# Optimization experiments

Measured on AMD Instinct MI355X. Metric: run time of the kernel, lower is better.

## Reference

```python
import jax, jax.numpy as jnp
import numpy as np

VOC_SIZE = 40
VOC_EMB = 32
LAYERS = [512, 1024, 2048]
LATENT = 512
START_TOK = 39
STOP_TOK = 0
MAX_STEPS = 50
BATCH = 64


def _gru_cell(x, h, Kg, bg, Kc, bc):
    # TF-style GRU: gates = sigmoid([x,h]@Kg + bg) -> (r, z);
    # cand = tanh([x, r*h]@Kc + bc); h' = z*h + (1-z)*cand
    out = h.shape[-1]
    v = jax.nn.sigmoid(jnp.concatenate([x, h], axis=-1) @ Kg + bg)
    r, z = v[..., :out], v[..., out:]
    c = jnp.tanh(jnp.concatenate([x, r * h], axis=-1) @ Kc + bc)
    return z * h + (1.0 - z) * c


def setup_inputs() -> dict:
    key = jax.random.key(0)
    ks = jax.random.split(key, 16)
    s = 0.05
    inp = {
        'input_vecs': jax.random.normal(ks[0], (BATCH, LATENT), jnp.float32),
        'emb': jax.random.normal(ks[1], (VOC_SIZE, VOC_EMB), jnp.float32) * s,
        'dense_W': jax.random.normal(ks[2], (LATENT, sum(LAYERS)), jnp.float32) * s,
        'dense_b': jnp.zeros((sum(LAYERS),), jnp.float32),
        'dec_W': jax.random.normal(ks[3], (LAYERS[2], VOC_SIZE), jnp.float32) * s,
    }
    ins = [VOC_EMB, LAYERS[0], LAYERS[1]]
    for i in range(3):
        ci = ins[i] + LAYERS[i]
        inp[f'Kg{i}'] = jax.random.normal(ks[4 + 4 * i], (ci, 2 * LAYERS[i]), jnp.float32) * s
        inp[f'bg{i}'] = jnp.ones((2 * LAYERS[i],), jnp.float32)  # TF GRU gate bias init 1.0
        inp[f'Kc{i}'] = jax.random.normal(ks[5 + 4 * i], (ci, LAYERS[i]), jnp.float32) * s
        inp[f'bc{i}'] = jnp.zeros((LAYERS[i],), jnp.float32)
    return inp


def reference(input_vecs, emb, dense_W, dense_b, dec_W,
              Kg0, bg0, Kc0, bc0, Kg1, bg1, Kc1, bc1, Kg2, bg2, Kc2, bc2):
    y = input_vecs @ dense_W + dense_b                       # [B, 3584]
    h0 = y[:, :LAYERS[0]]
    h1 = y[:, LAYERS[0]:LAYERS[0] + LAYERS[1]]
    h2 = y[:, LAYERS[0] + LAYERS[1]:]
    B = input_vecs.shape[0]
    x0 = jnp.broadcast_to(emb[START_TOK], (B, VOC_EMB))      # <s> embedding
    done0 = jnp.zeros((B,), bool)

    def step(carry, _):
        x, h0, h1, h2, done = carry
        n0 = _gru_cell(x, h0, Kg0, bg0, Kc0, bc0)
        n1 = _gru_cell(n0, h1, Kg1, bg1, Kc1, bc1)
        n2 = _gru_cell(n1, h2, Kg2, bg2, Kc2, bc2)
        logits = n2 @ dec_W                                  # [B, 40]
        idx = jnp.argmax(logits, axis=-1)                    # greedy sample
        d = done[:, None]
        # freeze state & outputs once a sequence emitted the stop token
        h0 = jnp.where(d, h0, n0)
        h1 = jnp.where(d, h1, n1)
        h2 = jnp.where(d, h2, n2)
        logits = jnp.where(d, 0.0, logits)
        tok = jnp.where(done, STOP_TOK, idx)
        x = jnp.where(d, x, emb[idx])
        done = done | (idx == STOP_TOK)
        return (x, h0, h1, h2, done), (tok, logits)

    _, (toks, logits) = jax.lax.scan(step, (x0, h0, h1, h2, done0), None, length=MAX_STEPS)
    # toks: [T, B] -> [B, T]; logits: [T, B, V] -> [B, T, V]
    return jnp.transpose(toks).astype(jnp.int32), jnp.transpose(logits, (1, 0, 2))
```

## Files before the change

kernel.cpp:

```cpp
#include <hip/hip_runtime.h>
#include <math.h>

#define NBLK 256
#define TPB  512
#define KB   128
#define ATS  65
#define LDSF 8448

#define GC 0
#define GG 512
#define RC 1024
#define RG 1056
#define AB 1088
__device__ unsigned g_sync[1120];
__device__ int g_tok[64];
__device__ int g_done[64];
__device__ __attribute__((aligned(16))) float g_hA[64 * 3584];
__device__ __attribute__((aligned(16))) float g_hB[64 * 3584];
__device__ __attribute__((aligned(16))) float g_v0h[64 * 1024];
__device__ __attribute__((aligned(16))) float g_v1a[64 * 2048];
__device__ __attribute__((aligned(16))) float g_v1b[64 * 2048];
__device__ __attribute__((aligned(16))) float g_c1x[64 * 1024];
__device__ __attribute__((aligned(16))) float g_v2a[64 * 4096];
__device__ __attribute__((aligned(16))) float g_v2b[64 * 4096];
__device__ __attribute__((aligned(16))) float g_cnd2a[64 * 2048];
__device__ __attribute__((aligned(16))) float g_cnd2b[64 * 2048];
__device__ __attribute__((aligned(16))) float g_c2x[64 * 2048];
__device__ __attribute__((aligned(16))) float g_ekg[40 * 1024];
__device__ __attribute__((aligned(16))) float g_ekc[40 * 512];

__device__ __forceinline__ float sigf(float x) { return 1.0f / (1.0f + __expf(-x)); }
__device__ __forceinline__ float tanhf_(float x) {
  float ax = fabsf(x);
  float e  = __expf(-2.0f * ax);
  float r  = (1.0f - e) / (1.0f + e);
  return copysignf(r, x);
}

__device__ __forceinline__ unsigned armw(unsigned* p, unsigned v) {
  return __hip_atomic_fetch_add(p, v, __ATOMIC_RELAXED, __HIP_MEMORY_SCOPE_AGENT);
}

struct AccP {
  const float* p; int lda;
  __device__ __forceinline__ float4 ld(int r, int k) const {
    return *(const float4*)(p + (size_t)r * lda + k);
  }
};
struct AccH {
  const float* pn; const float* po; int off; int cut;
  __device__ __forceinline__ float4 ld(int r, int k) const {
    const float* b = (k < cut) ? pn : po;
    return *(const float4*)(b + (size_t)r * 3584 + off + k);
  }
};
struct AccRH0 {
  const float* v; const float* ek; const int* tk; const float* h;
  __device__ __forceinline__ float4 ld(int r, int k) const {
    int t = tk[r];
    float4 a  = *(const float4*)(v + (size_t)r * 1024 + k);
    float4 b  = *(const float4*)(ek + (size_t)t * 1024 + k);
    float4 hh = *(const float4*)(h + (size_t)r * 3584 + k);
    return make_float4(sigf(a.x + b.x) * hh.x, sigf(a.y + b.y) * hh.y,
                       sigf(a.z + b.z) * hh.z, sigf(a.w + b.w) * hh.w);
  }
};
struct AccR1 {
  const float* va; const float* vb; const float* h;
  __device__ __forceinline__ float4 ld(int r, int k) const {
    float4 a  = *(const float4*)(va + (size_t)r * 2048 + k);
    float4 b  = *(const float4*)(vb + (size_t)r * 2048 + k);
    float4 hh = *(const float4*)(h + (size_t)r * 3584 + k);
    return make_float4(sigf(a.x + b.x) * hh.x, sigf(a.y + b.y) * hh.y,
                       sigf(a.z + b.z) * hh.z, sigf(a.w + b.w) * hh.w);
  }
};
struct AccR2 {
  const float* va; const float* vb; const float* h;
  __device__ __forceinline__ float4 ld(int r, int k) const {
    float4 a  = *(const float4*)(va + (size_t)r * 4096 + k);
    float4 b  = *(const float4*)(vb + (size_t)r * 4096 + k);
    float4 hh = *(const float4*)(h + (size_t)r * 3584 + k);
    return make_float4(sigf(a.x + b.x) * hh.x, sigf(a.y + b.y) * hh.y,
                       sigf(a.z + b.z) * hh.z, sigf(a.w + b.w) * hh.w);
  }
};
template <class Inner> struct AccOff {
  Inner in; int base;
  __device__ __forceinline__ float4 ld(int r, int k) const { return in.ld(r, base + k); }
};

#define FMA8(J, AJ) \
  acc[J][0] = fmaf(AJ, wv0.x, acc[J][0]); acc[J][1] = fmaf(AJ, wv0.y, acc[J][1]); \
  acc[J][2] = fmaf(AJ, wv0.z, acc[J][2]); acc[J][3] = fmaf(AJ, wv0.w, acc[J][3]); \
  acc[J][4] = fmaf(AJ, wv1.x, acc[J][4]); acc[J][5] = fmaf(AJ, wv1.y, acc[J][5]); \
  acc[J][6] = fmaf(AJ, wv1.z, acc[J][6]); acc[J][7] = fmaf(AJ, wv1.w, acc[J][7]);

template <class AF, class EF>
__device__ __forceinline__ void gemm32(const AF& A, const float* __restrict__ W,
                                       const int ldw, const int c0, const int K,
                                       float* __restrict__ lds, const EF& epi) {
  float* AT = lds;
  const int tid  = threadIdx.x;
  const int w    = tid >> 6;
  const int lane = tid & 63;
  const int rgrp = lane & 15;
  const int cg   = lane >> 4;
  const int sr = tid >> 3;
  const int sk = (tid & 7) * 16;

  float acc[4][8];
#pragma unroll
  for (int j = 0; j < 4; ++j)
#pragma unroll
    for (int e = 0; e < 8; ++e) acc[j][e] = 0.0f;

  float4 aR0 = A.ld(sr, sk + 0), aR1 = A.ld(sr, sk + 4);
  float4 aR2 = A.ld(sr, sk + 8), aR3 = A.ld(sr, sk + 12);

  const int NT = K / KB;
  const float* wbase = W + (size_t)w * ldw + c0 + cg * 8;

  for (int t = 0; t < NT; ++t) {
    __syncthreads();
    AT[(sk + 0)  * ATS + sr] = aR0.x;  AT[(sk + 1)  * ATS + sr] = aR0.y;
    AT[(sk + 2)  * ATS + sr] = aR0.z;  AT[(sk + 3)  * ATS + sr] = aR0.w;
    AT[(sk + 4)  * ATS + sr] = aR1.x;  AT[(sk + 5)  * ATS + sr] = aR1.y;
    AT[(sk + 6)  * ATS + sr] = aR1.z;  AT[(sk + 7)  * ATS + sr] = aR1.w;
    AT[(sk + 8)  * ATS + sr] = aR2.x;  AT[(sk + 9)  * ATS + sr] = aR2.y;
    AT[(sk + 10) * ATS + sr] = aR2.z;  AT[(sk + 11) * ATS + sr] = aR2.w;
    AT[(sk + 12) * ATS + sr] = aR3.x;  AT[(sk + 13) * ATS + sr] = aR3.y;
    AT[(sk + 14) * ATS + sr] = aR3.z;  AT[(sk + 15) * ATS + sr] = aR3.w;
    if (t + 1 < NT) {
      const int kb2 = (t + 1) * KB;
      aR0 = A.ld(sr, kb2 + sk + 0);  aR1 = A.ld(sr, kb2 + sk + 4);
      aR2 = A.ld(sr, kb2 + sk + 8);  aR3 = A.ld(sr, kb2 + sk + 12);
    }
    __syncthreads();
    const float* wrow = wbase + (size_t)t * KB * ldw;
    float4 wv0 = *(const float4*)wrow;
    float4 wv1 = *(const float4*)(wrow + 4);
#pragma unroll
    for (int i = 0; i < KB / 8; ++i) {
      const int kt = i * 8 + w;
      const float4 av = *(const float4*)&AT[kt * ATS + rgrp * 4];
      float4 nw0 = wv0, nw1 = wv1;
      if (i + 1 < KB / 8) {
        wrow += (size_t)8 * ldw;
        nw0 = *(const float4*)wrow;
        nw1 = *(const float4*)(wrow + 4);
      }
      FMA8(0, av.x) FMA8(1, av.y) FMA8(2, av.z) FMA8(3, av.w)
      wv0 = nw0; wv1 = nw1;
    }
  }
  float* red = lds;
  const int rb = (rgrp * 4) * 33 + cg * 8;
#define RED_STORE(S) { float* rp = red + (S) * 2112 + rb; \
  _Pragma("unroll") for (int j = 0; j < 4; ++j) _Pragma("unroll") \
    for (int e = 0; e < 8; ++e) rp[j * 33 + e] = acc[j][e]; }
#define RED_ADD(S) { float* rp = red + (S) * 2112 + rb; \
  _Pragma("unroll") for (int j = 0; j < 4; ++j) _Pragma("unroll") \
    for (int e = 0; e < 8; ++e) acc[j][e] += rp[j * 33 + e]; }
  __syncthreads();
  if (w >= 4) RED_STORE(w - 4);
  __syncthreads();
  if (w < 4) RED_ADD(w);
  __syncthreads();
  if (w == 2 || w == 3) RED_STORE(w - 2);
  __syncthreads();
  if (w < 2) RED_ADD(w);
  __syncthreads();
  if (w == 1) RED_STORE(0);
  __syncthreads();
  if (w == 0) {
    RED_ADD(0);
#pragma unroll
    for (int j = 0; j < 4; ++j)
#pragma unroll
      for (int e = 0; e < 8; ++e)
        epi(rgrp * 4 + j, c0 + cg * 8 + e, acc[j][e]);
  }
#undef RED_STORE
#undef RED_ADD
}

__global__ void __launch_bounds__(TPB, 2) decoder_kernel(
    const float* __restrict__ input_vecs, const float* __restrict__ emb,
    const float* __restrict__ dense_W, const float* __restrict__ dense_b,
    const float* __restrict__ dec_W,
    const float* __restrict__ Kg0, const float* __restrict__ bg0,
    const float* __restrict__ Kc0, const float* __restrict__ bc0,
    const float* __restrict__ Kg1, const float* __restrict__ bg1,
    const float* __restrict__ Kc1, const float* __restrict__ bc1,
    const float* __restrict__ Kg2, const float* __restrict__ bg2,
    const float* __restrict__ Kc2, const float* __restrict__ bc2,
    float* __restrict__ out) {
  __shared__ float lds[LDSF];
  __shared__ float lg[40];
  const int bid = blockIdx.x;
  const int tid = threadIdx.x;
  const int grp = bid >> 4;

  unsigned epoch = 0, gbase = 0, rbase = 0;
  if (tid == 0) {
    gbase = armw(&g_sync[GG + grp * 32], 0u);
    rbase = armw(&g_sync[RG], 0u);
  }
  auto gbar = [&]() {
    __syncthreads();
    if (tid == 0) {
      __builtin_amdgcn_fence(__ATOMIC_RELEASE, "agent");
      ++epoch;
      unsigned a = armw(&g_sync[GC + grp * 32], 1u) + 1u;
      if ((a & 15u) == 0u) {
        unsigned r = armw(&g_sync[RC], 1u) + 1u;
        if ((r & 15u) == 0u) armw(&g_sync[RG], 1u);
        unsigned polls = 0;
        while ((int)(armw(&g_sync[RG], 0u) - rbase) < (int)epoch) {
          __builtin_amdgcn_s_sleep(8);
          if ((++polls & 255u) == 0u) {
            if (polls > (1u << 20)) { armw(&g_sync[AB], 1u); break; }
            if (armw(&g_sync[AB], 0u) != 0u) break;
          }
        }
        armw(&g_sync[GG + grp * 32], 1u);
      } else {
        unsigned polls = 0;
        while ((int)(armw(&g_sync[GG + grp * 32], 0u) - gbase) < (int)epoch) {
          __builtin_amdgcn_s_sleep(8);
          if ((++polls & 255u) == 0u) {
            if (polls > (1u << 20)) { armw(&g_sync[AB], 1u); break; }
            if (armw(&g_sync[AB], 0u) != 0u) break;
          }
        }
      }
    }
    __syncthreads();
    __builtin_amdgcn_fence(__ATOMIC_ACQUIRE, "agent");
  };

  if (bid < 112) {
    AccP A{input_vecs, 512};
    auto epi = [&](int r, int c, float v) { g_hA[(size_t)r * 3584 + c] = v + dense_b[c]; };
    gemm32(A, dense_W, 3584, bid * 32, 512, lds, epi);
  }
  if (bid >= NBLK - 32) {
    int base = (bid - (NBLK - 32)) * 1920;
    for (int o = base + tid; o < base + 1920; o += TPB) {
      if (o < 40960) {
        int r = o >> 10, c = o & 1023;
        float s = 0.0f;
        for (int k = 0; k < 32; ++k) s += emb[r * 32 + k] * Kg0[k * 1024 + c];
        g_ekg[o] = s;
      } else {
        int o2 = o - 40960;
        int r = o2 >> 9, c = o2 & 511;
        float s = 0.0f;
        for (int k = 0; k < 32; ++k) s += emb[r * 32 + k] * Kc0[k * 512 + c];
        g_ekc[o2] = s;
      }
    }
  }
  if (bid == 128 && tid < 64) { g_tok[tid] = 39; g_done[tid] = 0; }
  gbar();

  if (bid < 32) {
    AccP A{g_hA, 3584};
    auto epi = [&](int r, int c, float v) { g_v0h[r * 1024 + c] = v + bg0[c]; };
    gemm32(A, Kg0 + 32 * 1024, 1024, bid * 32, 512, lds, epi);
  }
  gbar();

  for (int t = 0; t < 50; ++t) {
    const float* hOld = (t & 1) ? g_hB : g_hA;
    float*       hNew = (t & 1) ? g_hA : g_hB;

    if (bid < 16) {
      AccRH0 A{g_v0h, g_ekg, g_tok, hOld};
      auto epi = [&](int r, int c, float v) {
        int tk = g_tok[r];
        float cx = g_ekc[tk * 512 + c] + bc0[c];
        float z  = sigf(g_v0h[r * 1024 + 512 + c] + g_ekg[tk * 1024 + 512 + c]);
        float ho = hOld[(size_t)r * 3584 + c];
        hNew[(size_t)r * 3584 + c] = z * ho + (1.0f - z) * tanhf_(v + cx);
      };
      gemm32(A, Kc0 + 32 * 512, 512, bid * 32, 512, lds, epi);
    }
    gbar();

    if (bid < 128) {
      const int half = bid >> 6, ch = bid & 63;
      AccOff<AccH> A{{hNew, hOld, 0, 512}, half * 768};
      float* dst = half ? g_v1b : g_v1a;
      if (half == 0) {
        auto epi = [&](int r, int c, float v) { dst[r * 2048 + c] = v + bg1[c]; };
        gemm32(A, Kg1, 2048, ch * 32, 768, lds, epi);
      } else {
        auto epi = [&](int r, int c, float v) { dst[r * 2048 + c] = v; };
        gemm32(A, Kg1 + (size_t)768 * 2048, 2048, ch * 32, 768, lds, epi);
      }
    } else if (bid < 160) {
      AccP A{hNew, 3584};
      auto epi = [&](int r, int c, float v) { g_c1x[r * 1024 + c] = v + bc1[c]; };
      gemm32(A, Kc1, 1024, (bid - 128) * 32, 512, lds, epi);
    }
    gbar();

    if (bid < 32) {
      AccR1 A{g_v1a, g_v1b, hOld + 512};
      auto epi = [&](int r, int c, float v) {
        float z  = sigf(g_v1a[r * 2048 + 1024 + c] + g_v1b[r * 2048 + 1024 + c]);
        float cx = g_c1x[r * 1024 + c];
        float ho = hOld[(size_t)r * 3584 + 512 + c];
        hNew[(size_t)r * 3584 + 512 + c] = z * ho + (1.0f - z) * tanhf_(v + cx);
      };
      gemm32(A, Kc1 + (size_t)512 * 1024, 1024, bid * 32, 1024, lds, epi);
    }
    gbar();

    {
      const int half = bid >> 7, ch = bid & 127;
      AccOff<AccH> A{{hNew, hOld, 512, 1024}, half * 1536};
      if (half == 0) {
        auto epi = [&](int r, int c, float v) { g_v2a[(size_t)r * 4096 + c] = v + bg2[c]; };
        gemm32(A, Kg2, 4096, ch * 32, 1536, lds, epi);
      } else {
        auto epi = [&](int r, int c, float v) { g_v2b[(size_t)r * 4096 + c] = v; };
        gemm32(A, Kg2 + (size_t)1536 * 4096, 4096, ch * 32, 1536, lds, epi);
      }
    }
    gbar();

    if (bid < 128) {
      const int half = bid >> 6, ch = bid & 63;
      AccOff<AccR2> A{{g_v2a, g_v2b, hOld + 1536}, half * 1024};
      float* dst = half ? g_cnd2b : g_cnd2a;
      auto epi = [&](int r, int c, float v) { dst[r * 2048 + c] = v; };
      gemm32(A, Kc2 + (size_t)(1024 + half * 1024) * 2048, 2048, ch * 32, 1024, lds, epi);
    } else if (bid < 192) {
      AccP A{hNew + 512, 3584};
      auto epi = [&](int r, int c, float v) { g_c2x[r * 2048 + c] = v + bc2[c]; };
      gemm32(A, Kc2, 2048, (bid - 128) * 32, 1024, lds, epi);
    }
    gbar();

    if (bid < 64) {
      const int b = bid;
      float* h2row = lds;
      {
        const int c = tid * 4;
        float4 va = *(const float4*)&g_v2a[(size_t)b * 4096 + 2048 + c];
        float4 vb = *(const float4*)&g_v2b[(size_t)b * 4096 + 2048 + c];
        float4 ca = *(const float4*)&g_cnd2a[b * 2048 + c];
        float4 cb = *(const float4*)&g_cnd2b[b * 2048 + c];
        float4 cx = *(const float4*)&g_c2x[b * 2048 + c];
        float4 ho = *(const float4*)&hOld[(size_t)b * 3584 + 1536 + c];
        float4 r;
#define GRU2(comp) { float z = sigf(va.comp + vb.comp); \
        r.comp = z * ho.comp + (1.0f - z) * tanhf_(ca.comp + cb.comp + cx.comp); }
        GRU2(x) GRU2(y) GRU2(z) GRU2(w)
#undef GRU2
        *(float4*)&hNew[(size_t)b * 3584 + 1536 + c] = r;
        *(float4*)&h2row[c] = r;
      }
      __syncthreads();
      float acc = 0.0f;
      if (tid < 320) {
        const int v = tid >> 3, p = tid & 7;
        for (int i = 0; i < 64; ++i) {
          const int k = p * 4 + i * 32;
          float4 h = *(const float4*)&h2row[k];
          acc += h.x * dec_W[k * 40 + v] + h.y * dec_W[(k + 1) * 40 + v] +
                 h.z * dec_W[(k + 2) * 40 + v] + h.w * dec_W[(k + 3) * 40 + v];
        }
        acc += __shfl_xor(acc, 4);
        acc += __shfl_xor(acc, 2);
        acc += __shfl_xor(acc, 1);
        if (p == 0) lg[v] = acc;
      }
      __syncthreads();
      if (tid == 0) {
        int idx = 0; float best = lg[0];
        for (int v = 1; v < 40; ++v) { if (lg[v] > best) { best = lg[v]; idx = v; } }
        const int dn = g_done[b];
        out[b * 50 + t] = dn ? 0.0f : (float)idx;
        float* olg = out + 3200 + (size_t)(b * 50 + t) * 40;
        for (int v = 0; v < 40; ++v) olg[v] = dn ? 0.0f : lg[v];
        if (!dn) { g_tok[b] = idx; if (idx == 0) g_done[b] = 1; }
      }
    } else if (bid < 96) {
      AccP A{hNew, 3584};
      auto epi = [&](int r, int c, float v) { g_v0h[r * 1024 + c] = v + bg0[c]; };
      gemm32(A, Kg0 + 32 * 1024, 1024, (bid - 64) * 32, 512, lds, epi);
    }
    gbar();
  }
}

extern "C" void kernel_launch(void* const* d_in, const int* in_sizes, int n_in,
                              void* d_out, int out_size, void* d_ws, size_t ws_size,
                              hipStream_t stream) {
  (void)in_sizes; (void)n_in; (void)d_ws; (void)ws_size; (void)out_size;
  void* p0  = d_in[0];  void* p1  = d_in[1];  void* p2  = d_in[2];
  void* p3  = d_in[3];  void* p4  = d_in[4];  void* p5  = d_in[5];
  void* p6  = d_in[6];  void* p7  = d_in[7];  void* p8  = d_in[8];
  void* p9  = d_in[9];  void* p10 = d_in[10]; void* p11 = d_in[11];
  void* p12 = d_in[12]; void* p13 = d_in[13]; void* p14 = d_in[14];
  void* p15 = d_in[15]; void* p16 = d_in[16]; void* po  = d_out;
  void* args[] = {&p0, &p1, &p2, &p3, &p4, &p5, &p6, &p7, &p8,
                  &p9, &p10, &p11, &p12, &p13, &p14, &p15, &p16, &po};
  hipLaunchCooperativeKernel((const void*)decoder_kernel, dim3(NBLK), dim3(TPB),
                             args, 0, stream);
}
```

Before: 19.22 ms.

## Deepen weight prefetch to an 8-stage register ring in GEMM tiles

The GEMM inner loop now keeps eight k-slices of weights in registers as a rolling prefetch queue instead of a one-ahead prefetch, so more global weight loads are in flight and memory latency is better hidden. To make room, the k-tile shrinks to 64 with half as many activation staging loads per thread, and launch bounds drop to one block per CU so more registers are available. This trades occupancy and adds more LDS transposes and barriers per K for deeper memory-level parallelism.

```diff
diff --git a/kernel.cpp b/kernel.cpp
--- a/kernel.cpp
+++ b/kernel.cpp
@@ -3,7 +3,7 @@
 
 #define NBLK 256
 #define TPB  512
-#define KB   128
+#define KB   64
 #define ATS  65
 #define LDSF 8448
 
@@ -107,7 +107,7 @@
   const int rgrp = lane & 15;
   const int cg   = lane >> 4;
   const int sr = tid >> 3;
-  const int sk = (tid & 7) * 16;
+  const int sk = (tid & 7) * 8;
 
   float acc[4][8];
 #pragma unroll
@@ -115,51 +115,49 @@
 #pragma unroll
     for (int e = 0; e < 8; ++e) acc[j][e] = 0.0f;
 
-  float4 aR0 = A.ld(sr, sk + 0), aR1 = A.ld(sr, sk + 4);
-  float4 aR2 = A.ld(sr, sk + 8), aR3 = A.ld(sr, sk + 12);
+  const int S = K >> 3;
+  const float* wp = W + (size_t)w * ldw + c0 + cg * 8;
+  float4 wq0[8], wq1[8];
+#pragma unroll
+  for (int s = 0; s < 8; ++s) {
+    wq0[s] = *(const float4*)wp;
+    wq1[s] = *(const float4*)(wp + 4);
+    wp += (size_t)8 * ldw;
+  }
+
+  float4 a0 = A.ld(sr, sk), a1 = A.ld(sr, sk + 4);
 
   const int NT = K / KB;
-  const float* wbase = W + (size_t)w * ldw + c0 + cg * 8;
-
   for (int t = 0; t < NT; ++t) {
     __syncthreads();
-    AT[(sk + 0)  * ATS + sr] = aR0.x;  AT[(sk + 1)  * ATS + sr] = aR0.y;
-    AT[(sk + 2)  * ATS + sr] = aR0.z;  AT[(sk + 3)  * ATS + sr] = aR0.w;
-    AT[(sk + 4)  * ATS + sr] = aR1.x;  AT[(sk + 5)  * ATS + sr] = aR1.y;
-    AT[(sk + 6)  * ATS + sr] = aR1.z;  AT[(sk + 7)  * ATS + sr] = aR1.w;
-    AT[(sk + 8)  * ATS + sr] = aR2.x;  AT[(sk + 9)  * ATS + sr] = aR2.y;
-    AT[(sk + 10) * ATS + sr] = aR2.z;  AT[(sk + 11) * ATS + sr] = aR2.w;
-    AT[(sk + 12) * ATS + sr] = aR3.x;  AT[(sk + 13) * ATS + sr] = aR3.y;
-    AT[(sk + 14) * ATS + sr] = aR3.z;  AT[(sk + 15) * ATS + sr] = aR3.w;
+    AT[(sk + 0) * ATS + sr] = a0.x;  AT[(sk + 1) * ATS + sr] = a0.y;
+    AT[(sk + 2) * ATS + sr] = a0.z;  AT[(sk + 3) * ATS + sr] = a0.w;
+    AT[(sk + 4) * ATS + sr] = a1.x;  AT[(sk + 5) * ATS + sr] = a1.y;
+    AT[(sk + 6) * ATS + sr] = a1.z;  AT[(sk + 7) * ATS + sr] = a1.w;
     if (t + 1 < NT) {
-      const int kb2 = (t + 1) * KB;
-      aR0 = A.ld(sr, kb2 + sk + 0);  aR1 = A.ld(sr, kb2 + sk + 4);
-      aR2 = A.ld(sr, kb2 + sk + 8);  aR3 = A.ld(sr, kb2 + sk + 12);
+      a0 = A.ld(sr, (t + 1) * KB + sk);
+      a1 = A.ld(sr, (t + 1) * KB + sk + 4);
     }
     __syncthreads();
-    const float* wrow = wbase + (size_t)t * KB * ldw;
-    float4 wv0 = *(const float4*)wrow;
-    float4 wv1 = *(const float4*)(wrow + 4);
-#pragma unroll
-    for (int i = 0; i < KB / 8; ++i) {
-      const int kt = i * 8 + w;
-      const float4 av = *(const float4*)&AT[kt * ATS + rgrp * 4];
-      float4 nw0 = wv0, nw1 = wv1;
-      if (i + 1 < KB / 8) {
-        wrow += (size_t)8 * ldw;
-        nw0 = *(const float4*)wrow;
-        nw1 = *(const float4*)(wrow + 4);
+#pragma unroll
+    for (int i = 0; i < 8; ++i) {
+      const float4 av = *(const float4*)&AT[(i * 8 + w) * ATS + rgrp * 4];
+      const float4 wv0 = wq0[i];
+      const float4 wv1 = wq1[i];
+      if (t * 8 + i + 8 < S) {
+        wq0[i] = *(const float4*)wp;
+        wq1[i] = *(const float4*)(wp + 4);
+        wp += (size_t)8 * ldw;
       }
       FMA8(0, av.x) FMA8(1, av.y) FMA8(2, av.z) FMA8(3, av.w)
-      wv0 = nw0; wv1 = nw1;
     }
   }
   float* red = lds;
   const int rb = (rgrp * 4) * 33 + cg * 8;
-#define RED_STORE(S) { float* rp = red + (S) * 2112 + rb; \
+#define RED_STORE(Sx) { float* rp = red + (Sx) * 2112 + rb; \
   _Pragma("unroll") for (int j = 0; j < 4; ++j) _Pragma("unroll") \
     for (int e = 0; e < 8; ++e) rp[j * 33 + e] = acc[j][e]; }
-#define RED_ADD(S) { float* rp = red + (S) * 2112 + rb; \
+#define RED_ADD(Sx) { float* rp = red + (Sx) * 2112 + rb; \
   _Pragma("unroll") for (int j = 0; j < 4; ++j) _Pragma("unroll") \
     for (int e = 0; e < 8; ++e) acc[j][e] += rp[j * 33 + e]; }
   __syncthreads();
@@ -185,7 +183,7 @@
 #undef RED_ADD
 }
 
-__global__ void __launch_bounds__(TPB, 2) decoder_kernel(
+__global__ void __launch_bounds__(TPB, 1) decoder_kernel(
     const float* __restrict__ input_vecs, const float* __restrict__ emb,
     const float* __restrict__ dense_W, const float* __restrict__ dense_b,
     const float* __restrict__ dec_W,
```

After: 20.26 ms. +5.4%, slower.
